# Performance work log

Hardware: AMD Instinct MI355X
Metric: run time of the kernel (lower is better)

The kernel has to match this reference:

```python
import jax, jax.numpy as jnp
import numpy as np

B, NB, T, NC = 32, 55, 512, 8
D, H, E, K, DEPTH, FF = 128, 8, 8, 2, 4, 512  # embed, heads, experts, top_k, depth, ffn hidden=4*D
IN = NB * NC  # 440


def _ln(x, g, b, eps=1e-5):
    m = jnp.mean(x, axis=-1, keepdims=True)
    v = jnp.mean((x - m) ** 2, axis=-1, keepdims=True)
    return (x - m) / jnp.sqrt(v + eps) * g + b


def setup_inputs() -> dict:
    key = jax.random.key(0)
    ks = jax.random.split(key, 16)
    s = 0.02
    return {
        "x": jax.random.normal(ks[0], (B, NB, T, NC), jnp.float32),
        "proj_W": jax.random.normal(ks[1], (IN, D), jnp.float32) * s,
        "proj_b": jnp.zeros((D,), jnp.float32),
        "pos_embed": jax.random.normal(ks[2], (1, T, D), jnp.float32) * s,
        "ln1_g": jnp.ones((DEPTH, D), jnp.float32),
        "ln1_b": jnp.zeros((DEPTH, D), jnp.float32),
        "qkv_W": jax.random.normal(ks[3], (DEPTH, D, 3 * D), jnp.float32) * s,
        "qkv_b": jnp.zeros((DEPTH, 3 * D), jnp.float32),
        "out_W": jax.random.normal(ks[4], (DEPTH, D, D), jnp.float32) * s,
        "out_b": jnp.zeros((DEPTH, D), jnp.float32),
        "ln2_g": jnp.ones((DEPTH, D), jnp.float32),
        "ln2_b": jnp.zeros((DEPTH, D), jnp.float32),
        "gate_W": jax.random.normal(ks[5], (DEPTH, D, E), jnp.float32) * s,
        "w1": jax.random.normal(ks[6], (DEPTH, E, D, FF), jnp.float32) * s,
        "b1": jnp.zeros((DEPTH, E, FF), jnp.float32),
        "w2": jax.random.normal(ks[7], (DEPTH, E, FF, D), jnp.float32) * s,
        "b2": jnp.zeros((DEPTH, E, D), jnp.float32),
        "head_ln_g": jnp.ones((D,), jnp.float32),
        "head_ln_b": jnp.zeros((D,), jnp.float32),
        "head_W": jax.random.normal(ks[8], (D, 2), jnp.float32) * s,
        "head_b": jnp.zeros((2,), jnp.float32),
    }


def reference(x, proj_W, proj_b, pos_embed, ln1_g, ln1_b, qkv_W, qkv_b, out_W,
              out_b, ln2_g, ln2_b, gate_W, w1, b1, w2, b2, head_ln_g,
              head_ln_b, head_W, head_b):
    b, nb, t, nc = x.shape
    h = jnp.transpose(x, (0, 2, 1, 3)).reshape(b, t, nb * nc)  # [b,t,440]
    h = h @ proj_W + proj_b + pos_embed[:, :t, :]
    aux_total = jnp.float32(0.0)
    for i in range(DEPTH):
        # --- pre-LN multi-head self-attention ---
        z = _ln(h, ln1_g[i], ln1_b[i])
        qkv = z @ qkv_W[i] + qkv_b[i]
        q, k, v = jnp.split(qkv, 3, axis=-1)
        dh = D // H
        q = q.reshape(b, t, H, dh)
        k = k.reshape(b, t, H, dh)
        v = v.reshape(b, t, H, dh)
        att = jnp.einsum('bqhd,bkhd->bhqk', q, k) / jnp.sqrt(jnp.float32(dh))
        att = jax.nn.softmax(att, axis=-1)
        o = jnp.einsum('bhqk,bkhd->bqhd', att, v).reshape(b, t, D)
        h = h + o @ out_W[i] + out_b[i]
        # --- pre-LN top-k MoE FFN ---
        z = _ln(h, ln2_g[i], ln2_b[i])
        probs = jax.nn.softmax(z @ gate_W[i], axis=-1)  # [b,t,E]
        topv, topi = jax.lax.top_k(probs, K)
        wts = topv / jnp.sum(topv, axis=-1, keepdims=True)
        combine = jnp.sum(jax.nn.one_hot(topi, E, dtype=probs.dtype) * wts[..., None], axis=-2)  # [b,t,E]
        hid = jax.nn.gelu(jnp.einsum('btd,edf->btef', z, w1[i]) + b1[i])
        yexp = jnp.einsum('btef,efd->bted', hid, w2[i]) + b2[i]
        h = h + jnp.einsum('bte,bted->btd', combine, yexp)
        # Switch-style load-balancing auxiliary loss
        importance = probs.mean(axis=(0, 1))            # mean router prob per expert
        load = (combine > 0).astype(probs.dtype).mean(axis=(0, 1))  # dispatch fraction
        aux_total = aux_total + E * jnp.sum(importance * load)
    pooled = h.mean(axis=1)
    pooled = _ln(pooled, head_ln_g, head_ln_b)
    return pooled @ head_W + head_b, aux_total
```

## Files before the change

kernel.cpp:

```cpp
#include <hip/hip_runtime.h>
#include <hip/hip_bf16.h>
#include <cstdint>
#include <cstddef>

#define BT        16384
#define MAXASSIGN 33792
#define QSCALE    0.36067376022224085f

typedef __attribute__((ext_vector_type(8)))  short short8;
typedef __attribute__((ext_vector_type(4)))  short short4v;
typedef __attribute__((ext_vector_type(4)))  float f32x4;
typedef __attribute__((ext_vector_type(16))) float f32x16;

typedef const uint32_t __attribute__((address_space(1))) gas_u32;
typedef uint32_t __attribute__((address_space(3))) las_u32;

__device__ __forceinline__ void gload16(const void* g, void* l) {
    __builtin_amdgcn_global_load_lds((gas_u32*)g, (las_u32*)l, 16, 0, 0);
}

__device__ __forceinline__ float gelu_f(float x) {
    float u2l = (x + 0.044715f * x * x * x) * 2.3022081927f;
    float e = exp2f(u2l);
    float r = __builtin_amdgcn_rcpf(e + 1.0f);
    return x * e * r;
}

__device__ __forceinline__ unsigned pkbf(float a, float b) {
    __hip_bfloat16 ha = __float2bfloat16(a);
    __hip_bfloat16 hb = __float2bfloat16(b);
    unsigned short ua = *reinterpret_cast<unsigned short*>(&ha);
    unsigned short ub = *reinterpret_cast<unsigned short*>(&hb);
    return (unsigned)ua | ((unsigned)ub << 16);
}

__device__ __forceinline__ float bf2f(unsigned short u) {
    unsigned v = (unsigned)u << 16;
    return __uint_as_float(v);
}

__global__ void init_kernel(float* __restrict__ auxp, float* __restrict__ impc,
                            unsigned* __restrict__ zrow) {
    int tid = threadIdx.x;
    if (tid == 0) auxp[0] = 0.f;
    for (int u = tid; u < 4096; u += 256) impc[u] = 0.f;
    if (tid < 64) zrow[tid] = 0u;
}

__global__ __launch_bounds__(256) void transpose_kernel(const float* __restrict__ x,
                                                        __hip_bfloat16* __restrict__ xtb,
                                                        const float* __restrict__ projW,
                                                        __hip_bfloat16* __restrict__ projWt) {
    __shared__ unsigned tile[64][228];
    if (blockIdx.x >= 256) {
        int idx = (blockIdx.x - 256) * 256 + threadIdx.x;
        int k = idx % 448, n = idx / 448;
        projWt[idx] = __float2bfloat16(k < 440 ? projW[k * 128 + n] : 0.f);
        return;
    }
    const int b  = blockIdx.x >> 3;
    const int t0 = (blockIdx.x & 7) * 64;
    const int tid = threadIdx.x;
    tile[tid >> 2][220 + (tid & 3)] = 0u;
    const int tt  = tid >> 2;
    const int ncp = tid & 3;
    for (int nb = 0; nb < 55; ++nb) {
        const float2* src = (const float2*)(x + (((size_t)(b * 55 + nb)) * 512 + t0) * 8);
        float2 v = src[tid];
        tile[tt][nb * 4 + ncp] = pkbf(v.x, v.y);
    }
    __syncthreads();
#pragma unroll
    for (int u = 0; u < 14; ++u) {
        int idx = u * 256 + tid;
        int t = idx / 56, c = idx % 56;
        *(uint4*)(xtb + ((size_t)b * 512 + t0 + t) * 448 + c * 8) =
            *(const uint4*)&tile[t][c * 4];
    }
}

__global__ __launch_bounds__(256) void wconvt4_kernel(
    const float* __restrict__ qkvW, __hip_bfloat16* __restrict__ qkvWt_,
    const float* __restrict__ outW, __hip_bfloat16* __restrict__ outWt_,
    const float* __restrict__ w1i, __hip_bfloat16* __restrict__ w1o,
    const float* __restrict__ w2i, __hip_bfloat16* __restrict__ w2o)
{
    __shared__ float tile[64][65];
    const int bid = blockIdx.x;
    const float* in; __hip_bfloat16* out; int K, N, blk;
    if (bid < 48)       { in = qkvW; out = qkvWt_; K = 128; N = 384; blk = bid; }
    else if (bid < 64)  { in = outW; out = outWt_; K = 128; N = 128; blk = bid - 48; }
    else if (bid < 576) { in = w1i;  out = w1o;    K = 128; N = 512; blk = bid - 64; }
    else                { in = w2i;  out = w2o;    K = 512; N = 128; blk = bid - 576; }
    const int kt = K >> 6, nt = N >> 6;
    const int per = kt * nt;
    const int bb  = blk / per;
    const int rem = blk % per;
    const int k0  = (rem / nt) << 6;
    const int n0  = (rem % nt) << 6;
    const int tid = threadIdx.x;

    const float* src = in + ((size_t)bb * K + k0) * N + n0;
    int tk = tid >> 4;
    int tn = (tid & 15) * 4;
#pragma unroll
    for (int r = 0; r < 4; ++r) {
        float4 v = *(const float4*)(src + (size_t)(tk + r * 16) * N + tn);
        tile[tk + r * 16][tn]     = v.x;
        tile[tk + r * 16][tn + 1] = v.y;
        tile[tk + r * 16][tn + 2] = v.z;
        tile[tk + r * 16][tn + 3] = v.w;
    }
    __syncthreads();
    int on = tid >> 2;
    int ok = (tid & 3) * 16;
    unsigned pk[8];
#pragma unroll
    for (int u = 0; u < 8; ++u)
        pk[u] = pkbf(tile[ok + 2 * u][on], tile[ok + 2 * u + 1][on]);
    uint4* dst = (uint4*)(out + ((size_t)bb * N + n0 + on) * K + k0 + ok);
    dst[0] = (uint4){pk[0], pk[1], pk[2], pk[3]};
    dst[1] = (uint4){pk[4], pk[5], pk[6], pk[7]};
}

template<int MODE, int BM>
__global__ __launch_bounds__(256) void mm_kernel(
    const __hip_bfloat16* __restrict__ A, const __hip_bfloat16* __restrict__ Wt,
    const float* __restrict__ bias, const float* __restrict__ extra,
    void* __restrict__ Cout, int K, int N, int wstride,
    const int* __restrict__ moff, const int* __restrict__ atok,
    const float* __restrict__ awt)
{
    constexpr int FI = BM / 32;
    __shared__ short smem[16384];
    short* As = smem;
    short* Bs = smem + BM * 64;
    const int tid  = threadIdx.x;
    const int row0 = blockIdx.x * BM;
    const int col0 = blockIdx.y * 128;

    const float* bias2 = bias;
    int lim = 0;
    if constexpr (MODE == 3 || MODE == 4) {
        if (row0 >= moff[8]) return;
        int e = 0;
        while (moff[e + 1] <= row0) ++e;
        Wt    += (size_t)e * wstride;
        bias2  = bias + e * N;
        lim    = moff[e] + moff[9 + e];
    }

    const int wave = tid >> 6, lane = tid & 63;
    const int crow = tid >> 3;
    const int cc   = tid & 7;

    int srow[FI];
#pragma unroll
    for (int p = 0; p < FI; ++p) {
        int grow = row0 + p * 32 + crow;
        srow[p] = grow;
        if constexpr (MODE == 3)
            srow[p] = (grow < lim) ? atok[grow] : BT;
    }

    f32x4 acc[FI][4];
#pragma unroll
    for (int i = 0; i < FI; ++i)
#pragma unroll
        for (int j = 0; j < 4; ++j) acc[i][j] = (f32x4){0.f, 0.f, 0.f, 0.f};

    const int wm = (wave >> 1) * (BM / 2), wn = (wave & 1) * 64;
    const int lr = lane & 15, q = lane >> 4;

    for (int k0 = 0; k0 < K; k0 += 64) {
#pragma unroll
        for (int p = 0; p < FI; ++p) {
            int row = p * 32 + crow;
            int sc  = (cc ^ (row & 7)) << 3;
            short* la = &As[(p * 32 + wave * 8) * 64];
            gload16(A + (size_t)srow[p] * K + k0 + sc, la);
        }
#pragma unroll
        for (int p = 0; p < 4; ++p) {
            int row = p * 32 + crow;
            int sc  = (cc ^ (row & 7)) << 3;
            short* lb = &Bs[(p * 32 + wave * 8) * 64];
            gload16(Wt + (size_t)(col0 + row) * K + k0 + sc, lb);
        }
        __syncthreads();
#pragma unroll
        for (int s = 0; s < 2; ++s) {
            short8 af[FI], bf[4];
#pragma unroll
            for (int f = 0; f < FI; ++f) {
                int m = wm + f * 16 + lr;
                af[f] = *(const short8*)&As[(m * 8 + ((s * 4 + q) ^ (m & 7))) * 8];
            }
#pragma unroll
            for (int f = 0; f < 4; ++f) {
                int n = wn + f * 16 + lr;
                bf[f] = *(const short8*)&Bs[(n * 8 + ((s * 4 + q) ^ (n & 7))) * 8];
            }
#pragma unroll
            for (int i = 0; i < FI; ++i)
#pragma unroll
                for (int j = 0; j < 4; ++j)
                    acc[i][j] = __builtin_amdgcn_mfma_f32_16x16x32_bf16(
                        bf[j], af[i], acc[i][j], 0, 0, 0);
        }
        __syncthreads();
    }

    float4 b4[4];
#pragma unroll
    for (int j = 0; j < 4; ++j)
        b4[j] = *(const float4*)&bias2[col0 + wn + j * 16 + q * 4];

    if constexpr (MODE == 3 || MODE == 4 || MODE == 5) {
        const bool qsc = (MODE == 5) && (col0 == 0);
#pragma unroll
        for (int i = 0; i < FI; ++i) {
            int trow = wm + i * 16 + lr;
            float aw = 1.f;
            if constexpr (MODE == 4) aw = awt[row0 + trow];
#pragma unroll
            for (int j = 0; j < 4; ++j) {
                int cb = wn + j * 16 + q * 4;
                float v0 = acc[i][j][0] + b4[j].x;
                float v1 = acc[i][j][1] + b4[j].y;
                float v2 = acc[i][j][2] + b4[j].z;
                float v3 = acc[i][j][3] + b4[j].w;
                if constexpr (MODE == 3) {
                    v0 = gelu_f(v0); v1 = gelu_f(v1);
                    v2 = gelu_f(v2); v3 = gelu_f(v3);
                }
                if constexpr (MODE == 4) {
                    v0 *= aw; v1 *= aw; v2 *= aw; v3 *= aw;
                }
                if (qsc) { v0 *= QSCALE; v1 *= QSCALE; v2 *= QSCALE; v3 *= QSCALE; }
                uint2 pk = {pkbf(v0, v1), pkbf(v2, v3)};
                int ch = cb >> 3;
                *(uint2*)((char*)smem + trow * 256 + ((ch ^ (trow & 7)) << 4)
                          + ((cb & 7) << 1)) = pk;
            }
        }
        __syncthreads();
        __hip_bfloat16* outb = (__hip_bfloat16*)Cout;
        constexpr int TPR = 256 / BM;
        constexpr int CPT = 16 / TPR;
        int rrow = tid / TPR;
        if constexpr (MODE == 3 || MODE == 4) {
            size_t rb = (size_t)(row0 + rrow) * N + col0;
#pragma unroll
            for (int u = 0; u < CPT; ++u) {
                int c = (tid % TPR) * CPT + u;
                uint4 d = *(const uint4*)((char*)smem + rrow * 256
                                          + ((c ^ (rrow & 7)) << 4));
                *(uint4*)(outb + rb + c * 8) = d;
            }
        } else {
            size_t pbase = (size_t)(col0 >> 7) * 8 * BT * 16;
#pragma unroll
            for (int u = 0; u < CPT; ++u) {
                int c = (tid % TPR) * CPT + u;
                uint4 d = *(const uint4*)((char*)smem + rrow * 256
                                          + ((c ^ (rrow & 7)) << 4));
                size_t dst = pbase + ((size_t)(c >> 1) * BT + row0 + rrow) * 16
                           + (c & 1) * 8;
                *(uint4*)(outb + dst) = d;
            }
        }
    } else {
        float* outf = (float*)Cout;
        constexpr int HP = BM / 64;
        for (int h = 0; h < HP; ++h) {
            if (HP == 1 || (wm >> 6) == h) {
#pragma unroll
                for (int i = 0; i < FI; ++i) {
                    int trow = (wm & 63) + i * 16 + lr;
#pragma unroll
                    for (int j = 0; j < 4; ++j) {
                        int cb = wn + j * 16 + q * 4;
                        f32x4 v = acc[i][j];
                        v[0] += b4[j].x; v[1] += b4[j].y;
                        v[2] += b4[j].z; v[3] += b4[j].w;
                        int ch = cb >> 2;
                        *(f32x4*)((char*)smem + trow * 512
                                  + ((ch ^ (trow & 7)) << 4)) = v;
                    }
                }
            }
            __syncthreads();
            {
                int rrow = tid >> 2;
                int grow = row0 + h * 64 + rrow;
                size_t rb = (size_t)grow * N + col0;
#pragma unroll
                for (int u = 0; u < 8; ++u) {
                    int c = (tid & 3) * 8 + u;
                    f32x4 d = *(const f32x4*)((char*)smem + rrow * 512
                                              + ((c ^ (rrow & 7)) << 4));
                    int gcol = col0 + c * 4;
                    if constexpr (MODE == 0) {
                        float4 p = *(const float4*)&extra[(grow & 511) * 128 + gcol];
                        d[0] += p.x; d[1] += p.y; d[2] += p.z; d[3] += p.w;
                    } else if constexpr (MODE == 2) {
                        float4 p = *(const float4*)&extra[rb + c * 4];
                        d[0] += p.x; d[1] += p.y; d[2] += p.z; d[3] += p.w;
                    }
                    *(f32x4*)&outf[rb + c * 4] = d;
                }
            }
            __syncthreads();
        }
    }
}

__global__ __launch_bounds__(256) void ln_kernel(const float* __restrict__ x,
                                                 const float* __restrict__ g,
                                                 const float* __restrict__ b,
                                                 __hip_bfloat16* __restrict__ zbf) {
    int wave = threadIdx.x >> 6, lane = threadIdx.x & 63;
    size_t row = (size_t)blockIdx.x * 4 + wave;
    const float* xr = x + row * 128;
    float a0 = xr[lane], a1 = xr[lane + 64];
    float s = a0 + a1;
#pragma unroll
    for (int off = 32; off > 0; off >>= 1) s += __shfl_xor(s, off);
    float mean = s * (1.f / 128.f);
    float d0 = a0 - mean, d1 = a1 - mean;
    float v = d0 * d0 + d1 * d1;
#pragma unroll
    for (int off = 32; off > 0; off >>= 1) v += __shfl_xor(v, off);
    float inv = rsqrtf(v * (1.f / 128.f) + 1e-5f);
    zbf[row * 128 + lane]      = __float2bfloat16(d0 * inv * g[lane] + b[lane]);
    zbf[row * 128 + lane + 64] = __float2bfloat16(d1 * inv * g[lane + 64] + b[lane + 64]);
}

__global__ __launch_bounds__(1024) void attn_kernel(const __hip_bfloat16* __restrict__ qkv,
                                                    __hip_bfloat16* __restrict__ o) {
    __shared__ short Ks[512 * 24];
    __shared__ short Vt[17 * 520];
    const int hh = blockIdx.x, b = blockIdx.y;
    const int tid = threadIdx.x;
    const __hip_bfloat16* Qh = qkv + ((size_t)(0 * 8 + hh) * BT + b * 512) * 16;
    const __hip_bfloat16* Kh = qkv + ((size_t)(1 * 8 + hh) * BT + b * 512) * 16;
    const __hip_bfloat16* Vh = qkv + ((size_t)(2 * 8 + hh) * BT + b * 512) * 16;

    if (tid < 512) {
        int r = tid;
        const uint4* ksrc = (const uint4*)(Kh + (size_t)r * 16);
        uint4 k0 = ksrc[0], k1 = ksrc[1];
        *(uint4*)&Ks[r * 24 + 0] = k0;
        *(uint4*)&Ks[r * 24 + 8] = k1;
    } else {
        int r = tid - 512;
        const uint4* vsrc = (const uint4*)(Vh + (size_t)r * 16);
        uint4 v0 = vsrc[0], v1 = vsrc[1];
        unsigned vv[8] = {v0.x, v0.y, v0.z, v0.w, v1.x, v1.y, v1.z, v1.w};
#pragma unroll
        for (int c = 0; c < 8; ++c) {
            Vt[(2 * c)     * 520 + r] = (short)(vv[c] & 0xffff);
            Vt[(2 * c + 1) * 520 + r] = (short)(vv[c] >> 16);
        }
        Vt[16 * 520 + r] = (short)0x3F80;
    }
    __syncthreads();

    const int wave = tid >> 6, lane = tid & 63;
    const int lm = lane & 31, lh = lane >> 5;
    const int qrow0 = wave * 32;

    short8 qf = *(const short8*)(Qh + (size_t)(qrow0 + lm) * 16 + lh * 8);

    f32x16 accO;
#pragma unroll
    for (int r = 0; r < 16; ++r) accO[r] = 0.f;

    for (int kc = 0; kc < 16; ++kc) {
        short8 kf = *(const short8*)&Ks[(kc * 32 + lm) * 24 + lh * 8];
        int vr = (lm < 16) ? lm : 16;
        const short* vb2 = &Vt[vr * 520 + kc * 32];
        short4v va  = *(const short4v*)(vb2 + 4 * lh);
        short4v vbq = *(const short4v*)(vb2 + 8 + 4 * lh);
        short4v vc  = *(const short4v*)(vb2 + 16 + 4 * lh);
        short4v vd  = *(const short4v*)(vb2 + 24 + 4 * lh);
        short8 vf0, vf1;
#pragma unroll
        for (int j = 0; j < 4; ++j) {
            vf0[j] = va[j];  vf0[4 + j] = vbq[j];
            vf1[j] = vc[j];  vf1[4 + j] = vd[j];
        }
        f32x16 st;
#pragma unroll
        for (int r = 0; r < 16; ++r) st[r] = 0.f;
        st = __builtin_amdgcn_mfma_f32_32x32x16_bf16(kf, qf, st, 0, 0, 0);
        short8 pf0, pf1;
#pragma unroll
        for (int r = 0; r < 8; ++r) {
            pf0[r] = (short)(__float_as_uint(exp2f(st[r]))     >> 16);
            pf1[r] = (short)(__float_as_uint(exp2f(st[8 + r])) >> 16);
        }
        accO = __builtin_amdgcn_mfma_f32_32x32x16_bf16(pf0, vf0, accO, 0, 0, 0);
        accO = __builtin_amdgcn_mfma_f32_32x32x16_bf16(pf1, vf1, accO, 0, 0, 0);
    }

#pragma unroll
    for (int r = 0; r < 16; ++r) {
        float val = accO[r];
        float s = __shfl(val, (lane & 32) + 16);
        if (lm < 16) {
            int qr = qrow0 + (r & 3) + 8 * (r >> 2) + 4 * lh;
            o[((size_t)b * 512 + qr) * 128 + hh * 16 + lm] = __float2bfloat16(val / s);
        }
    }
}

__global__ __launch_bounds__(256) void ln2gate_kernel(
    const float* __restrict__ x, const float* __restrict__ g, const float* __restrict__ b,
    const float* __restrict__ gW, __hip_bfloat16* __restrict__ zbf,
    int* __restrict__ topi, float* __restrict__ topw,
    float* __restrict__ impS, int* __restrict__ cntS)
{
    __shared__ float simp[8];
    __shared__ int scnt[8];
    const int tid = threadIdx.x;
    if (tid < 8) { simp[tid] = 0.f; scnt[tid] = 0; }
    __syncthreads();
    const int wave = tid >> 6, lane = tid & 63;
    const size_t row = (size_t)blockIdx.x * 4 + wave;
    const float* xr = x + row * 128;
    float a0 = xr[lane], a1 = xr[lane + 64];
    float s = a0 + a1;
#pragma unroll
    for (int off = 32; off > 0; off >>= 1) s += __shfl_xor(s, off);
    float mean = s * (1.f / 128.f);
    float d0 = a0 - mean, d1 = a1 - mean;
    float v = d0 * d0 + d1 * d1;
#pragma unroll
    for (int off = 32; off > 0; off >>= 1) v += __shfl_xor(v, off);
    float inv = rsqrtf(v * (1.f / 128.f) + 1e-5f);
    float o0 = d0 * inv * g[lane] + b[lane];
    float o1 = d1 * inv * g[lane + 64] + b[lane + 64];
    zbf[row * 128 + lane]      = __float2bfloat16(o0);
    zbf[row * 128 + lane + 64] = __float2bfloat16(o1);
    float4 gA = *(const float4*)&gW[lane * 8];
    float4 gB = *(const float4*)&gW[lane * 8 + 4];
    float4 gC = *(const float4*)&gW[(lane + 64) * 8];
    float4 gD = *(const float4*)&gW[(lane + 64) * 8 + 4];
    float lg[8];
    lg[0] = o0 * gA.x + o1 * gC.x;  lg[1] = o0 * gA.y + o1 * gC.y;
    lg[2] = o0 * gA.z + o1 * gC.z;  lg[3] = o0 * gA.w + o1 * gC.w;
    lg[4] = o0 * gB.x + o1 * gD.x;  lg[5] = o0 * gB.y + o1 * gD.y;
    lg[6] = o0 * gB.z + o1 * gD.z;  lg[7] = o0 * gB.w + o1 * gD.w;
#pragma unroll
    for (int e = 0; e < 8; ++e)
#pragma unroll
        for (int off = 32; off > 0; off >>= 1) lg[e] += __shfl_xor(lg[e], off);
    if (lane == 0) {
        float p[8];
        float mx = lg[0];
#pragma unroll
        for (int k = 1; k < 8; ++k) mx = fmaxf(mx, lg[k]);
        float ssum = 0.f;
#pragma unroll
        for (int k = 0; k < 8; ++k) { p[k] = expf(lg[k] - mx); ssum += p[k]; }
        float pinv = 1.f / ssum;
#pragma unroll
        for (int k = 0; k < 8; ++k) p[k] *= pinv;
        int i0 = 0; float v0 = p[0];
#pragma unroll
        for (int k = 1; k < 8; ++k) if (p[k] > v0) { v0 = p[k]; i0 = k; }
        int i1 = -1; float v1 = -1.f;
#pragma unroll
        for (int k = 0; k < 8; ++k) if (k != i0 && p[k] > v1) { v1 = p[k]; i1 = k; }
        float wsum = v0 + v1;
        topi[row * 2] = i0;  topi[row * 2 + 1] = i1;
        topw[row * 2] = v0 / wsum;  topw[row * 2 + 1] = v1 / wsum;
#pragma unroll
        for (int k = 0; k < 8; ++k) atomicAdd(&simp[k], p[k]);
        atomicAdd(&scnt[i0], 1); atomicAdd(&scnt[i1], 1);
    }
    __syncthreads();
    if (tid < 8) {
        int slot = (blockIdx.x >> 6) * 8 + tid;
        atomicAdd(&impS[slot], simp[tid]);
        atomicAdd(&cntS[slot], scnt[tid]);
    }
}

__global__ __launch_bounds__(256) void scatter_kernel(
    const int* __restrict__ topi, const float* __restrict__ topw,
    const int* __restrict__ cntS, const float* __restrict__ impS,
    int* __restrict__ atok, float* __restrict__ awt, int* __restrict__ tokpos,
    int* __restrict__ moffw, float* __restrict__ aux)
{
    __shared__ int lcnt[8];
    __shared__ int lbase[8];
    __shared__ int csum[8];
    __shared__ float isum[8];
    const int tid = threadIdx.x;
    const int blk = blockIdx.x;
    if (tid < 64) {
        int e = tid & 7, grp = tid >> 3;
        int ct = 0, cp = 0; float im = 0.f;
        for (int g = 0; g < 8; ++g) {
            int sl = grp * 8 + g;
            int vv = cntS[sl * 8 + e];
            ct += vv;
            cp += (sl < blk) ? vv : 0;
            im += impS[sl * 8 + e];
        }
#pragma unroll
        for (int off = 32; off >= 8; off >>= 1) {
            ct += __shfl_down(ct, off);
            cp += __shfl_down(cp, off);
            im += __shfl_down(im, off);
        }
        if (tid < 8) { csum[tid] = ct; isum[tid] = im; lbase[tid] = cp; lcnt[tid] = 0; }
    }
    __syncthreads();
    if (tid < 8) {
        int t = 0;
        for (int k = 0; k < tid; ++k) t += (csum[k] + 127) & ~127;
        lbase[tid] += t;
    }
    if (blk == 0 && tid == 64) {
        int t = 0; float s = 0.f;
        for (int k = 0; k < 8; ++k) {
            int ck = csum[k];
            moffw[k] = t;
            moffw[9 + k] = ck;
            t += (ck + 127) & ~127;
            s += (isum[k] * (1.f / 16384.f)) * ((float)ck * (1.f / 16384.f));
        }
        moffw[8] = t;
        aux[0] += 8.f * s;
    }
    __syncthreads();
    const int token = blk * 256 + tid;
    const int e0 = topi[token * 2], e1 = topi[token * 2 + 1];
    const float w0 = topw[token * 2], w1 = topw[token * 2 + 1];
    const int l0 = atomicAdd(&lcnt[e0], 1);
    const int l1 = atomicAdd(&lcnt[e1], 1);
    const int p0 = lbase[e0] + l0;
    const int p1 = lbase[e1] + l1;
    atok[p0] = token;  awt[p0] = w0;  tokpos[token * 2]     = p0;
    atok[p1] = token;  awt[p1] = w1;  tokpos[token * 2 + 1] = p1;
}

__global__ __launch_bounds__(256) void combine_ln_kernel(
    const __hip_bfloat16* __restrict__ yw, const int* __restrict__ tokpos,
    float* __restrict__ h, const float* __restrict__ g, const float* __restrict__ b,
    __hip_bfloat16* __restrict__ zbf)
{
    const int tid = threadIdx.x;
    const int wave = tid >> 6, lane = tid & 63;
    const size_t row = (size_t)blockIdx.x * 4 + wave;
    const int p0 = tokpos[row * 2], p1 = tokpos[row * 2 + 1];
    const unsigned short* y0 = (const unsigned short*)(yw + (size_t)p0 * 128);
    const unsigned short* y1 = (const unsigned short*)(yw + (size_t)p1 * 128);
    float a0 = h[row * 128 + lane]      + bf2f(y0[lane])      + bf2f(y1[lane]);
    float a1 = h[row * 128 + lane + 64] + bf2f(y0[lane + 64]) + bf2f(y1[lane + 64]);
    h[row * 128 + lane]      = a0;
    h[row * 128 + lane + 64] = a1;
    if (zbf) {
        float s = a0 + a1;
#pragma unroll
        for (int off = 32; off > 0; off >>= 1) s += __shfl_xor(s, off);
        float mean = s * (1.f / 128.f);
        float d0 = a0 - mean, d1 = a1 - mean;
        float v = d0 * d0 + d1 * d1;
#pragma unroll
        for (int off = 32; off > 0; off >>= 1) v += __shfl_xor(v, off);
        float inv = rsqrtf(v * (1.f / 128.f) + 1e-5f);
        zbf[row * 128 + lane]      = __float2bfloat16(d0 * inv * g[lane] + b[lane]);
        zbf[row * 128 + lane + 64] = __float2bfloat16(d1 * inv * g[lane + 64] + b[lane + 64]);
    }
}

__global__ __launch_bounds__(1024) void head_kernel(const float* __restrict__ h,
                                                    const float* __restrict__ g,
                                                    const float* __restrict__ bb,
                                                    const float* __restrict__ hW,
                                                    const float* __restrict__ hb,
                                                    const float* __restrict__ aux,
                                                    float* __restrict__ out) {
    __shared__ float part[8][128];
    __shared__ float red[128];
    __shared__ float pl[128];
    int b = blockIdx.x, tid = threadIdx.x;
    int c = tid & 127, w = tid >> 7;
    float s = 0.f;
    for (int t = w; t < 512; t += 8) s += h[((size_t)b * 512 + t) * 128 + c];
    part[w][c] = s;
    __syncthreads();
    float pooled = 0.f;
    if (tid < 128) {
#pragma unroll
        for (int k = 0; k < 8; ++k) pooled += part[k][tid];
        pooled *= (1.f / 512.f);
        red[tid] = pooled;
    }
    __syncthreads();
    for (int st = 64; st > 0; st >>= 1) { if (tid < st) red[tid] += red[tid + st]; __syncthreads(); }
    float mean = red[0] * (1.f / 128.f);
    __syncthreads();
    float d = pooled - mean;
    if (tid < 128) red[tid] = d * d;
    __syncthreads();
    for (int st = 64; st > 0; st >>= 1) { if (tid < st) red[tid] += red[tid + st]; __syncthreads(); }
    float var = red[0] * (1.f / 128.f);
    if (tid < 128) pl[tid] = d / sqrtf(var + 1e-5f) * g[tid] + bb[tid];
    __syncthreads();
    if (tid < 2) {
        float acc = hb[tid];
        for (int k = 0; k < 128; ++k) acc += pl[k] * hW[k * 2 + tid];
        out[b * 2 + tid] = acc;
    }
    if (b == 0 && tid == 0) out[64] = aux[0];
}

extern "C" void kernel_launch(void* const* d_in, const int* in_sizes, int n_in,
                              void* d_out, int out_size, void* d_ws, size_t ws_size,
                              hipStream_t stream) {
    (void)in_sizes; (void)n_in; (void)out_size; (void)ws_size;
    const float* x      = (const float*)d_in[0];
    const float* proj_W = (const float*)d_in[1];
    const float* proj_b = (const float*)d_in[2];
    const float* pos    = (const float*)d_in[3];
    const float* ln1_g  = (const float*)d_in[4];
    const float* ln1_b  = (const float*)d_in[5];
    const float* qkv_W  = (const float*)d_in[6];
    const float* qkv_b  = (const float*)d_in[7];
    const float* out_W  = (const float*)d_in[8];
    const float* out_b  = (const float*)d_in[9];
    const float* ln2_g  = (const float*)d_in[10];
    const float* ln2_b  = (const float*)d_in[11];
    const float* gate_W = (const float*)d_in[12];
    const float* w1     = (const float*)d_in[13];
    const float* b1     = (const float*)d_in[14];
    const float* w2     = (const float*)d_in[15];
    const float* b2     = (const float*)d_in[16];
    const float* hl_g   = (const float*)d_in[17];
    const float* hl_b   = (const float*)d_in[18];
    const float* head_W = (const float*)d_in[19];
    const float* head_b = (const float*)d_in[20];
    float* outp = (float*)d_out;

    float* ws = (float*)d_ws;
    size_t off = 0;
    auto alloc = [&](size_t n) { float* p = ws + off; off += (n + 63) & ~(size_t)63; return p; };
    float* hidbf_f = alloc((size_t)MAXASSIGN * 256);
    float* h       = alloc((size_t)BT * 128);
    float* zbf_f   = alloc((size_t)(BT + 1) * 64);
    float* qkvbf_f = alloc((size_t)BT * 192);
    float* obbf_f  = alloc((size_t)BT * 64);
    float* yw      = alloc((size_t)MAXASSIGN * 64);
    float* projWt_f= alloc(128 * 448 / 2);
    float* qkvWt_f = alloc(4 * 384 * 128 / 2);
    float* outWt_f = alloc(4 * 128 * 128 / 2);
    float* w1t_f   = alloc((size_t)32 * 512 * 128 / 2);
    float* w2t_f   = alloc((size_t)32 * 128 * 512 / 2);
    float* topw    = alloc(32768);
    float* awt     = alloc(MAXASSIGN);
    float* impc    = alloc(4096);
    float* auxp    = alloc(1);
    int* topi      = (int*)alloc(32768);
    int* atok      = (int*)alloc(MAXASSIGN);
    int* tokpos    = (int*)alloc(32768);
    int* moff      = (int*)alloc(32);

    __hip_bfloat16* hidbf  = (__hip_bfloat16*)hidbf_f;
    __hip_bfloat16* xtb    = (__hip_bfloat16*)hidbf_f;
    __hip_bfloat16* zbf    = (__hip_bfloat16*)zbf_f;
    __hip_bfloat16* qkvbf  = (__hip_bfloat16*)qkvbf_f;
    __hip_bfloat16* obbf   = (__hip_bfloat16*)obbf_f;
    __hip_bfloat16* ywb    = (__hip_bfloat16*)yw;
    __hip_bfloat16* projWt = (__hip_bfloat16*)projWt_f;
    __hip_bfloat16* qkvWt  = (__hip_bfloat16*)qkvWt_f;
    __hip_bfloat16* outWt  = (__hip_bfloat16*)outWt_f;
    __hip_bfloat16* w1t    = (__hip_bfloat16*)w1t_f;
    __hip_bfloat16* w2t    = (__hip_bfloat16*)w2t_f;

    init_kernel<<<1, 256, 0, stream>>>(auxp, impc,
                                       (unsigned*)((char*)zbf + (size_t)BT * 256));

    transpose_kernel<<<480, 256, 0, stream>>>(x, xtb, proj_W, projWt);
    wconvt4_kernel<<<1088, 256, 0, stream>>>(qkv_W, qkvWt, out_W, outWt,
                                             w1, w1t, w2, w2t);

    mm_kernel<0, 64><<<dim3(256, 1), 256, 0, stream>>>(
        xtb, projWt, proj_b, pos, h, 448, 128, 0, nullptr, nullptr, nullptr);
    ln_kernel<<<4096, 256, 0, stream>>>(h, ln1_g, ln1_b, zbf);

    for (int i = 0; i < 4; ++i) {
        float* impS = impc + (size_t)i * 1024;
        int*   cntS = (int*)(impc + (size_t)i * 1024 + 512);
        mm_kernel<5, 64><<<dim3(256, 3), 256, 0, stream>>>(
            zbf, qkvWt + (size_t)i * 384 * 128, qkv_b + i * 384, nullptr, qkvbf,
            128, 384, 0, nullptr, nullptr, nullptr);
        attn_kernel<<<dim3(8, 32), 1024, 0, stream>>>(qkvbf, obbf);
        mm_kernel<2, 64><<<dim3(256, 1), 256, 0, stream>>>(
            obbf, outWt + (size_t)i * 128 * 128, out_b + i * 128, h, h,
            128, 128, 0, nullptr, nullptr, nullptr);
        ln2gate_kernel<<<4096, 256, 0, stream>>>(h, ln2_g + i * 128, ln2_b + i * 128,
                                                 gate_W + (size_t)i * 128 * 8, zbf,
                                                 topi, topw, impS, cntS);
        scatter_kernel<<<64, 256, 0, stream>>>(topi, topw, cntS, impS,
                                               atok, awt, tokpos, moff, auxp);
        mm_kernel<3, 64><<<dim3(528, 4), 256, 0, stream>>>(
            zbf, w1t + (size_t)i * 8 * 512 * 128, b1 + (size_t)i * 8 * 512, nullptr,
            hidbf, 128, 512, 512 * 128, moff, atok, awt);
        mm_kernel<4, 64><<<dim3(528, 1), 256, 0, stream>>>(
            hidbf, w2t + (size_t)i * 8 * 128 * 512, b2 + (size_t)i * 8 * 128, nullptr,
            ywb, 512, 128, 128 * 512, moff, atok, awt);
        combine_ln_kernel<<<4096, 256, 0, stream>>>(ywb, tokpos, h,
                                                    ln1_g + (i + 1 < 4 ? (i + 1) * 128 : 0),
                                                    ln1_b + (i + 1 < 4 ? (i + 1) * 128 : 0),
                                                    (i < 3) ? zbf : (__hip_bfloat16*)nullptr);
    }
    head_kernel<<<32, 1024, 0, stream>>>(h, hl_g, hl_b, head_W, head_b, auxp, outp);
}
```

Measured before the change: 599.6 us.

## Fuse MoE expert FFN up/down projections into one kernel keeping hidden in LDS

Replaces the two grouped expert GEMM launches (w1 with GELU, then w2 with routing-weight scaling) with a single moe_kernel. Each 64-row block gathers its routed token rows once, computes the 512-wide hidden activation in 128-column chunks, applies GELU and stores it to shared memory, then immediately accumulates the w2 product. This removes the global write and re-read of the large bf16 hidden buffer and one launch per layer. In exchange, each block runs the 512-wide hidden dimension serially, so the grid has fewer blocks than the old four-way column split. It also uses more shared memory and has no prefetch overlap of weight loads.

```diff
diff --git a/kernel.cpp b/kernel.cpp
--- a/kernel.cpp
+++ b/kernel.cpp
@@ -127,9 +127,7 @@
 __global__ __launch_bounds__(256) void mm_kernel(
     const __hip_bfloat16* __restrict__ A, const __hip_bfloat16* __restrict__ Wt,
     const float* __restrict__ bias, const float* __restrict__ extra,
-    void* __restrict__ Cout, int K, int N, int wstride,
-    const int* __restrict__ moff, const int* __restrict__ atok,
-    const float* __restrict__ awt)
+    void* __restrict__ Cout, int K, int N)
 {
     constexpr int FI = BM / 32;
     __shared__ short smem[16384];
@@ -139,29 +137,9 @@
     const int row0 = blockIdx.x * BM;
     const int col0 = blockIdx.y * 128;
 
-    const float* bias2 = bias;
-    int lim = 0;
-    if constexpr (MODE == 3 || MODE == 4) {
-        if (row0 >= moff[8]) return;
-        int e = 0;
-        while (moff[e + 1] <= row0) ++e;
-        Wt    += (size_t)e * wstride;
-        bias2  = bias + e * N;
-        lim    = moff[e] + moff[9 + e];
-    }
-
     const int wave = tid >> 6, lane = tid & 63;
     const int crow = tid >> 3;
     const int cc   = tid & 7;
-
-    int srow[FI];
-#pragma unroll
-    for (int p = 0; p < FI; ++p) {
-        int grow = row0 + p * 32 + crow;
-        srow[p] = grow;
-        if constexpr (MODE == 3)
-            srow[p] = (grow < lim) ? atok[grow] : BT;
-    }
 
     f32x4 acc[FI][4];
 #pragma unroll
@@ -178,7 +156,7 @@
             int row = p * 32 + crow;
             int sc  = (cc ^ (row & 7)) << 3;
             short* la = &As[(p * 32 + wave * 8) * 64];
-            gload16(A + (size_t)srow[p] * K + k0 + sc, la);
+            gload16(A + (size_t)(row0 + row) * K + k0 + sc, la);
         }
 #pragma unroll
         for (int p = 0; p < 4; ++p) {
@@ -214,15 +192,13 @@
     float4 b4[4];
 #pragma unroll
     for (int j = 0; j < 4; ++j)
-        b4[j] = *(const float4*)&bias2[col0 + wn + j * 16 + q * 4];
-
-    if constexpr (MODE == 3 || MODE == 4 || MODE == 5) {
-        const bool qsc = (MODE == 5) && (col0 == 0);
+        b4[j] = *(const float4*)&bias[col0 + wn + j * 16 + q * 4];
+
+    if constexpr (MODE == 5) {
+        const bool qsc = (col0 == 0);
 #pragma unroll
         for (int i = 0; i < FI; ++i) {
             int trow = wm + i * 16 + lr;
-            float aw = 1.f;
-            if constexpr (MODE == 4) aw = awt[row0 + trow];
 #pragma unroll
             for (int j = 0; j < 4; ++j) {
                 int cb = wn + j * 16 + q * 4;
@@ -230,13 +206,6 @@
                 float v1 = acc[i][j][1] + b4[j].y;
                 float v2 = acc[i][j][2] + b4[j].z;
                 float v3 = acc[i][j][3] + b4[j].w;
-                if constexpr (MODE == 3) {
-                    v0 = gelu_f(v0); v1 = gelu_f(v1);
-                    v2 = gelu_f(v2); v3 = gelu_f(v3);
-                }
-                if constexpr (MODE == 4) {
-                    v0 *= aw; v1 *= aw; v2 *= aw; v3 *= aw;
-                }
                 if (qsc) { v0 *= QSCALE; v1 *= QSCALE; v2 *= QSCALE; v3 *= QSCALE; }
                 uint2 pk = {pkbf(v0, v1), pkbf(v2, v3)};
                 int ch = cb >> 3;
@@ -249,69 +218,237 @@
         constexpr int TPR = 256 / BM;
         constexpr int CPT = 16 / TPR;
         int rrow = tid / TPR;
-        if constexpr (MODE == 3 || MODE == 4) {
-            size_t rb = (size_t)(row0 + rrow) * N + col0;
-#pragma unroll
-            for (int u = 0; u < CPT; ++u) {
-                int c = (tid % TPR) * CPT + u;
-                uint4 d = *(const uint4*)((char*)smem + rrow * 256
-                                          + ((c ^ (rrow & 7)) << 4));
-                *(uint4*)(outb + rb + c * 8) = d;
-            }
-        } else {
-            size_t pbase = (size_t)(col0 >> 7) * 8 * BT * 16;
-#pragma unroll
-            for (int u = 0; u < CPT; ++u) {
-                int c = (tid % TPR) * CPT + u;
-                uint4 d = *(const uint4*)((char*)smem + rrow * 256
-                                          + ((c ^ (rrow & 7)) << 4));
-                size_t dst = pbase + ((size_t)(c >> 1) * BT + row0 + rrow) * 16
-                           + (c & 1) * 8;
-                *(uint4*)(outb + dst) = d;
-            }
+        size_t pbase = (size_t)(col0 >> 7) * 8 * BT * 16;
+#pragma unroll
+        for (int u = 0; u < CPT; ++u) {
+            int c = (tid % TPR) * CPT + u;
+            uint4 d = *(const uint4*)((char*)smem + rrow * 256
+                                      + ((c ^ (rrow & 7)) << 4));
+            size_t dst = pbase + ((size_t)(c >> 1) * BT + row0 + rrow) * 16
+                       + (c & 1) * 8;
+            *(uint4*)(outb + dst) = d;
         }
     } else {
         float* outf = (float*)Cout;
-        constexpr int HP = BM / 64;
-        for (int h = 0; h < HP; ++h) {
-            if (HP == 1 || (wm >> 6) == h) {
-#pragma unroll
-                for (int i = 0; i < FI; ++i) {
-                    int trow = (wm & 63) + i * 16 + lr;
-#pragma unroll
-                    for (int j = 0; j < 4; ++j) {
-                        int cb = wn + j * 16 + q * 4;
-                        f32x4 v = acc[i][j];
-                        v[0] += b4[j].x; v[1] += b4[j].y;
-                        v[2] += b4[j].z; v[3] += b4[j].w;
-                        int ch = cb >> 2;
-                        *(f32x4*)((char*)smem + trow * 512
-                                  + ((ch ^ (trow & 7)) << 4)) = v;
-                    }
+#pragma unroll
+        for (int i = 0; i < FI; ++i) {
+            int trow = wm + i * 16 + lr;
+#pragma unroll
+            for (int j = 0; j < 4; ++j) {
+                int cb = wn + j * 16 + q * 4;
+                f32x4 v = acc[i][j];
+                v[0] += b4[j].x; v[1] += b4[j].y;
+                v[2] += b4[j].z; v[3] += b4[j].w;
+                int ch = cb >> 2;
+                *(f32x4*)((char*)smem + trow * 512
+                          + ((ch ^ (trow & 7)) << 4)) = v;
+            }
+        }
+        __syncthreads();
+        {
+            int rrow = tid >> 2;
+            int grow = row0 + rrow;
+            size_t rb = (size_t)grow * N + col0;
+#pragma unroll
+            for (int u = 0; u < 8; ++u) {
+                int c = (tid & 3) * 8 + u;
+                f32x4 d = *(const f32x4*)((char*)smem + rrow * 512
+                                          + ((c ^ (rrow & 7)) << 4));
+                int gcol = col0 + c * 4;
+                if constexpr (MODE == 0) {
+                    float4 p = *(const float4*)&extra[(grow & 511) * 128 + gcol];
+                    d[0] += p.x; d[1] += p.y; d[2] += p.z; d[3] += p.w;
+                } else if constexpr (MODE == 2) {
+                    float4 p = *(const float4*)&extra[rb + c * 4];
+                    d[0] += p.x; d[1] += p.y; d[2] += p.z; d[3] += p.w;
                 }
+                *(f32x4*)&outf[rb + c * 4] = d;
+            }
+        }
+        __syncthreads();
+    }
+}
+
+__global__ __launch_bounds__(256) void moe_kernel(
+    const __hip_bfloat16* __restrict__ zbf, const __hip_bfloat16* __restrict__ w1t,
+    const float* __restrict__ b1, const __hip_bfloat16* __restrict__ w2t,
+    const float* __restrict__ b2, __hip_bfloat16* __restrict__ yout,
+    const int* __restrict__ moff, const int* __restrict__ atok,
+    const float* __restrict__ awt)
+{
+    __shared__ short smem[24576];
+    short* zA = smem;
+    short* Bs = smem + 8192;
+    short* hA = smem + 16384;
+    const int tid  = threadIdx.x;
+    const int row0 = blockIdx.x * 64;
+    if (row0 >= moff[8]) return;
+    int e = 0;
+    while (moff[e + 1] <= row0) ++e;
+    const __hip_bfloat16* W1 = w1t + (size_t)e * 512 * 128;
+    const __hip_bfloat16* W2 = w2t + (size_t)e * 128 * 512;
+    const float* bb1 = b1 + e * 512;
+    const float* bb2 = b2 + e * 128;
+    const int lim = moff[e] + moff[9 + e];
+
+    const int wave = tid >> 6, lane = tid & 63;
+    const int crow = tid >> 3;
+    const int cc   = tid & 7;
+
+    int srow[2];
+#pragma unroll
+    for (int p = 0; p < 2; ++p) {
+        int grow = row0 + p * 32 + crow;
+        srow[p] = (grow < lim) ? atok[grow] : BT;
+    }
+
+#pragma unroll
+    for (int ks = 0; ks < 2; ++ks)
+#pragma unroll
+        for (int p = 0; p < 2; ++p) {
+            int row = p * 32 + crow;
+            int sc  = (cc ^ (row & 7)) << 3;
+            gload16(zbf + (size_t)srow[p] * 128 + ks * 64 + sc,
+                    &zA[ks * 4096 + (p * 32 + wave * 8) * 64]);
+        }
+
+    const int wm = (wave >> 1) * 32, wn = (wave & 1) * 64;
+    const int lr = lane & 15, q = lane >> 4;
+
+    f32x4 acc2[2][4];
+#pragma unroll
+    for (int i = 0; i < 2; ++i)
+#pragma unroll
+        for (int j = 0; j < 4; ++j) acc2[i][j] = (f32x4){0.f, 0.f, 0.f, 0.f};
+
+    __syncthreads();
+
+    for (int f0 = 0; f0 < 4; ++f0) {
+        f32x4 acc1[2][4];
+#pragma unroll
+        for (int i = 0; i < 2; ++i)
+#pragma unroll
+            for (int j = 0; j < 4; ++j) acc1[i][j] = (f32x4){0.f, 0.f, 0.f, 0.f};
+
+#pragma unroll
+        for (int ks = 0; ks < 2; ++ks) {
+#pragma unroll
+            for (int p = 0; p < 4; ++p) {
+                int row = p * 32 + crow;
+                int sc  = (cc ^ (row & 7)) << 3;
+                gload16(W1 + (size_t)(f0 * 128 + row) * 128 + ks * 64 + sc,
+                        &Bs[(p * 32 + wave * 8) * 64]);
             }
             __syncthreads();
-            {
-                int rrow = tid >> 2;
-                int grow = row0 + h * 64 + rrow;
-                size_t rb = (size_t)grow * N + col0;
-#pragma unroll
-                for (int u = 0; u < 8; ++u) {
-                    int c = (tid & 3) * 8 + u;
-                    f32x4 d = *(const f32x4*)((char*)smem + rrow * 512
-                                              + ((c ^ (rrow & 7)) << 4));
-                    int gcol = col0 + c * 4;
-                    if constexpr (MODE == 0) {
-                        float4 p = *(const float4*)&extra[(grow & 511) * 128 + gcol];
-                        d[0] += p.x; d[1] += p.y; d[2] += p.z; d[3] += p.w;
-                    } else if constexpr (MODE == 2) {
-                        float4 p = *(const float4*)&extra[rb + c * 4];
-                        d[0] += p.x; d[1] += p.y; d[2] += p.z; d[3] += p.w;
-                    }
-                    *(f32x4*)&outf[rb + c * 4] = d;
+#pragma unroll
+            for (int s = 0; s < 2; ++s) {
+                short8 af[2], bf[4];
+#pragma unroll
+                for (int f = 0; f < 2; ++f) {
+                    int m = wm + f * 16 + lr;
+                    af[f] = *(const short8*)&zA[ks * 4096
+                            + (m * 8 + ((s * 4 + q) ^ (m & 7))) * 8];
                 }
+#pragma unroll
+                for (int f = 0; f < 4; ++f) {
+                    int n = wn + f * 16 + lr;
+                    bf[f] = *(const short8*)&Bs[(n * 8 + ((s * 4 + q) ^ (n & 7))) * 8];
+                }
+#pragma unroll
+                for (int i = 0; i < 2; ++i)
+#pragma unroll
+                    for (int j = 0; j < 4; ++j)
+                        acc1[i][j] = __builtin_amdgcn_mfma_f32_16x16x32_bf16(
+                            bf[j], af[i], acc1[i][j], 0, 0, 0);
             }
             __syncthreads();
+        }
+
+#pragma unroll
+        for (int i = 0; i < 2; ++i) {
+            int trow = wm + i * 16 + lr;
+#pragma unroll
+            for (int j = 0; j < 4; ++j) {
+                int cb = wn + j * 16 + q * 4;
+                float4 g4 = *(const float4*)&bb1[f0 * 128 + cb];
+                float v0 = gelu_f(acc1[i][j][0] + g4.x);
+                float v1 = gelu_f(acc1[i][j][1] + g4.y);
+                float v2 = gelu_f(acc1[i][j][2] + g4.z);
+                float v3 = gelu_f(acc1[i][j][3] + g4.w);
+                uint2 pk = {pkbf(v0, v1), pkbf(v2, v3)};
+                int s2 = cb >> 6, kl = cb & 63, ch = kl >> 3;
+                *(uint2*)((char*)hA + s2 * 8192 + trow * 128
+                          + ((ch ^ (trow & 7)) << 4) + ((kl & 7) << 1)) = pk;
+            }
+        }
+        __syncthreads();
+
+#pragma unroll
+        for (int ks2 = 0; ks2 < 2; ++ks2) {
+#pragma unroll
+            for (int p = 0; p < 4; ++p) {
+                int row = p * 32 + crow;
+                int sc  = (cc ^ (row & 7)) << 3;
+                gload16(W2 + (size_t)row * 512 + f0 * 128 + ks2 * 64 + sc,
+                        &Bs[(p * 32 + wave * 8) * 64]);
+            }
+            __syncthreads();
+#pragma unroll
+            for (int s = 0; s < 2; ++s) {
+                short8 af[2], bf[4];
+#pragma unroll
+                for (int f = 0; f < 2; ++f) {
+                    int m = wm + f * 16 + lr;
+                    af[f] = *(const short8*)&hA[ks2 * 4096
+                            + (m * 8 + ((s * 4 + q) ^ (m & 7))) * 8];
+                }
+#pragma unroll
+                for (int f = 0; f < 4; ++f) {
+                    int n = wn + f * 16 + lr;
+                    bf[f] = *(const short8*)&Bs[(n * 8 + ((s * 4 + q) ^ (n & 7))) * 8];
+                }
+#pragma unroll
+                for (int i = 0; i < 2; ++i)
+#pragma unroll
+                    for (int j = 0; j < 4; ++j)
+                        acc2[i][j] = __builtin_amdgcn_mfma_f32_16x16x32_bf16(
+                            bf[j], af[i], acc2[i][j], 0, 0, 0);
+            }
+            __syncthreads();
+        }
+    }
+
+    float4 b4[4];
+#pragma unroll
+    for (int j = 0; j < 4; ++j)
+        b4[j] = *(const float4*)&bb2[wn + j * 16 + q * 4];
+#pragma unroll
+    for (int i = 0; i < 2; ++i) {
+        int trow = wm + i * 16 + lr;
+        float aw = awt[row0 + trow];
+#pragma unroll
+        for (int j = 0; j < 4; ++j) {
+            int cb = wn + j * 16 + q * 4;
+            float v0 = (acc2[i][j][0] + b4[j].x) * aw;
+            float v1 = (acc2[i][j][1] + b4[j].y) * aw;
+            float v2 = (acc2[i][j][2] + b4[j].z) * aw;
+            float v3 = (acc2[i][j][3] + b4[j].w) * aw;
+            uint2 pk = {pkbf(v0, v1), pkbf(v2, v3)};
+            int ch = cb >> 3;
+            *(uint2*)((char*)Bs + trow * 256 + ((ch ^ (trow & 7)) << 4)
+                      + ((cb & 7) << 1)) = pk;
+        }
+    }
+    __syncthreads();
+    {
+        int rrow = tid >> 2;
+        size_t rb = (size_t)(row0 + rrow) * 128;
+#pragma unroll
+        for (int u = 0; u < 4; ++u) {
+            int c = (tid & 3) * 4 + u;
+            uint4 d = *(const uint4*)((char*)Bs + rrow * 256
+                                      + ((c ^ (rrow & 7)) << 4));
+            *(uint4*)(yout + rb + c * 8) = d;
         }
     }
 }
@@ -651,7 +788,7 @@
     float* ws = (float*)d_ws;
     size_t off = 0;
     auto alloc = [&](size_t n) { float* p = ws + off; off += (n + 63) & ~(size_t)63; return p; };
-    float* hidbf_f = alloc((size_t)MAXASSIGN * 256);
+    float* xtb_f   = alloc((size_t)BT * 224);
     float* h       = alloc((size_t)BT * 128);
     float* zbf_f   = alloc((size_t)(BT + 1) * 64);
     float* qkvbf_f = alloc((size_t)BT * 192);
@@ -671,8 +808,7 @@
     int* tokpos    = (int*)alloc(32768);
     int* moff      = (int*)alloc(32);
 
-    __hip_bfloat16* hidbf  = (__hip_bfloat16*)hidbf_f;
-    __hip_bfloat16* xtb    = (__hip_bfloat16*)hidbf_f;
+    __hip_bfloat16* xtb    = (__hip_bfloat16*)xtb_f;
     __hip_bfloat16* zbf    = (__hip_bfloat16*)zbf_f;
     __hip_bfloat16* qkvbf  = (__hip_bfloat16*)qkvbf_f;
     __hip_bfloat16* obbf   = (__hip_bfloat16*)obbf_f;
@@ -691,7 +827,7 @@
                                              w1, w1t, w2, w2t);
 
     mm_kernel<0, 64><<<dim3(256, 1), 256, 0, stream>>>(
-        xtb, projWt, proj_b, pos, h, 448, 128, 0, nullptr, nullptr, nullptr);
+        xtb, projWt, proj_b, pos, h, 448, 128);
     ln_kernel<<<4096, 256, 0, stream>>>(h, ln1_g, ln1_b, zbf);
 
     for (int i = 0; i < 4; ++i) {
@@ -699,22 +835,20 @@
         int*   cntS = (int*)(impc + (size_t)i * 1024 + 512);
         mm_kernel<5, 64><<<dim3(256, 3), 256, 0, stream>>>(
             zbf, qkvWt + (size_t)i * 384 * 128, qkv_b + i * 384, nullptr, qkvbf,
-            128, 384, 0, nullptr, nullptr, nullptr);
+            128, 384);
         attn_kernel<<<dim3(8, 32), 1024, 0, stream>>>(qkvbf, obbf);
         mm_kernel<2, 64><<<dim3(256, 1), 256, 0, stream>>>(
             obbf, outWt + (size_t)i * 128 * 128, out_b + i * 128, h, h,
-            128, 128, 0, nullptr, nullptr, nullptr);
+            128, 128);
         ln2gate_kernel<<<4096, 256, 0, stream>>>(h, ln2_g + i * 128, ln2_b + i * 128,
                                                  gate_W + (size_t)i * 128 * 8, zbf,
                                                  topi, topw, impS, cntS);
         scatter_kernel<<<64, 256, 0, stream>>>(topi, topw, cntS, impS,
                                                atok, awt, tokpos, moff, auxp);
-        mm_kernel<3, 64><<<dim3(528, 4), 256, 0, stream>>>(
-            zbf, w1t + (size_t)i * 8 * 512 * 128, b1 + (size_t)i * 8 * 512, nullptr,
-            hidbf, 128, 512, 512 * 128, moff, atok, awt);
-        mm_kernel<4, 64><<<dim3(528, 1), 256, 0, stream>>>(
-            hidbf, w2t + (size_t)i * 8 * 128 * 512, b2 + (size_t)i * 8 * 128, nullptr,
-            ywb, 512, 128, 128 * 512, moff, atok, awt);
+        moe_kernel<<<528, 256, 0, stream>>>(
+            zbf, w1t + (size_t)i * 8 * 512 * 128, b1 + (size_t)i * 8 * 512,
+            w2t + (size_t)i * 8 * 128 * 512, b2 + (size_t)i * 8 * 128,
+            ywb, moff, atok, awt);
         combine_ln_kernel<<<4096, 256, 0, stream>>>(ywb, tokpos, h,
                                                     ln1_g + (i + 1 < 4 ? (i + 1) * 128 : 0),
                                                     ln1_b + (i + 1 < 4 ? (i + 1) * 128 : 0),
```

Result: faster. 557.9 us (-7.0%).
